# Optimization experiments

Hardware: AMD Instinct MI355X
Metric: run time of the kernel (lower is better)

The kernel has to match this reference:

```python
import jax, jax.numpy as jnp
import numpy as np
from jax import lax

A = 20          # alphabet size (input_size)
L = 512         # max_seq_length
CH = 8          # conv channels
N_LAYERS = 9    # log2(512) conv+pool stages


def setup_inputs() -> dict:
    key = jax.random.key(0)
    ks = jax.random.split(key, 6)
    B = 1024
    idx = jax.random.randint(ks[0], (B, L), 0, A)
    lens = jax.random.randint(ks[1], (B,), L // 4, L + 1)
    masks = jnp.arange(L)[None, :] < lens[:, None]            # [B, L] bool
    # one-hot sequences, zeroed at padded positions (so nonzero() skips them)
    x = jax.nn.one_hot(idx, A, dtype=jnp.float32) * masks[..., None].astype(jnp.float32)
    blosum = jax.random.normal(ks[2], (A, A), jnp.float32)
    blosum = (blosum + blosum.T) * 0.5                        # symmetric like BLOSUM
    lpm = blosum                                              # trainable copy
    pm = jnp.clip(blosum, 0.0)                                # clamp(min=0) constant
    std = jnp.ones((1,), jnp.float32)                         # Gaussian std for row decay
    w0 = jax.random.normal(ks[3], (CH, 1, 3), jnp.float32) * 0.3
    ws = jax.random.normal(ks[4], (N_LAYERS - 1, CH, CH, 3), jnp.float32) * 0.2
    return {"x": x, "masks": masks, "lpm": lpm, "pm": pm, "std": std, "w0": w0, "ws": ws}


def _shift_pos(m, k):
    # target index clamp(s + k, max=L-1): shift right by k, boundary index L-1
    # collects any source in the last k+1 positions (set semantics -> OR).
    head = jnp.zeros(m.shape[:-1] + (k,), dtype=bool)
    body = m[..., : L - k - 1]                                # targets k .. L-2
    last = jnp.any(m[..., L - 1 - k:], axis=-1, keepdims=True)
    return jnp.concatenate([head, body, last], axis=-1)


def _shift_neg(m, k):
    # target index clamp(s - k, min=0)
    first = jnp.any(m[..., : k + 1], axis=-1, keepdims=True)
    body = m[..., k + 1:]                                     # targets 1 .. L-1-k
    tail = jnp.zeros(m.shape[:-1] + (k,), dtype=bool)
    return jnp.concatenate([first, body, tail], axis=-1)


def _column(nz, lpm, pm):
    # Banded substitution scatter: each one-hot row i writes V[i, r] into row r
    # at the same (batch, seq) position. Original nested index_put loops collapse
    # to a single 20x20 matrix V applied via einsum (one-hot => no collisions).
    ii = jnp.arange(A)[:, None]
    rr = jnp.arange(A)[None, :]
    M = jnp.clip(lpm, 0.001, 1.0) * pm
    # up-writes: j in 1..18-i => i < r <= 18 ; down-writes: j in 1..i => r < i
    V = jnp.where((rr > ii) & (rr <= A - 2), M, 0.0) + jnp.where(rr < ii, M.T, 0.0)
    return jnp.einsum('bis,ir->brs', nz, V)


def _row(m, std):
    # Gaussian positional decay: writes exp(-k^2/(2 std^2)) at seq offsets +-k,
    # k = 1,2,3 in order (later k overwrites earlier at clamp collisions).
    row = jnp.zeros(m.shape, jnp.float32)
    for k in (1, 2, 3):
        mk = _shift_pos(m, k) | _shift_neg(m, k)
        vk = jnp.exp(-(k * k) / (2.0 * std * std))[0]
        row = jnp.where(mk, vk, row)
    return row


def _conv1d(h, w):
    # Conv1d(kernel=3, stride=1, pad=1, no bias)
    return lax.conv_general_dilated(h, w, (1,), [(1, 1)],
                                    dimension_numbers=('NCH', 'OIH', 'NCH'))


def _avgpool2(h):
    N, C, Lh = h.shape
    return h.reshape(N, C, Lh // 2, 2).mean(-1)


def reference(x, masks, lpm, pm, std, w0, ws):
    B = x.shape[0]
    xp = jnp.transpose(x, (0, 2, 1))          # [B, 20, L]
    m = xp != 0
    nz = m.astype(xp.dtype)
    h = xp + _column(nz, lpm, pm) + _row(m, std)
    h = h.reshape(B * A, 1, L)
    h = _avgpool2(_conv1d(h, w0))
    for i in range(N_LAYERS - 1):
        h = _avgpool2(_conv1d(h, ws[i]))
    return h.squeeze(-1).reshape(B, A, -1)    # [B, 20, 8]
```

## Files before the change

kernel.cpp:

```cpp
#include <hip/hip_runtime.h>
#include <math.h>

#define LSEQ 512
#define NA 20
#define NCH 8
#define SV 33

__global__ __launch_bounds__(256) void wf_vt_kernel(
    const float* __restrict__ w0,
    const float* __restrict__ wsg,
    const float* __restrict__ lpm,
    const float* __restrict__ pm,
    float* __restrict__ wf,
    float* __restrict__ vtn)
{
    const int t = threadIdx.x;

    if (blockIdx.x == NCH) {
        for (int o = t; o < NA * NA; o += 256) {
            int j = o / NA, a = o % NA;
            float v = 0.f;
            if (a > j && a <= NA - 2)
                v += fminf(fmaxf(lpm[j * NA + a], 0.001f), 1.0f) * pm[j * NA + a];
            if (a < j)
                v += fminf(fmaxf(lpm[a * NA + j], 0.001f), 1.0f) * pm[a * NA + j];
            vtn[o] = v;
        }
        return;
    }

    const int r = blockIdx.x;

    __shared__ float gA[NCH * 256];
    __shared__ float gB[NCH * 256];
    __shared__ float4 s_e[NCH * NCH];

    if (t < NCH) gA[t * 256] = (t == r) ? 1.f : 0.f;
    __syncthreads();

    int P = 1;
    for (int step = 0; step < 8; ++step) {
        const int li = 7 - step;
        if (t < 64) {
            const int co = t >> 3, ci = t & 7;
            const float* wp = wsg + li * 192 + co * 24 + ci * 3;
            const float a0 = wp[0], a1 = wp[1], a2 = wp[2];
            s_e[co * 8 + ci] = make_float4(a0 + a1, a2, a1 + a2, a0);
        }
        __syncthreads();
        const float* gi = (step & 1) ? gB : gA;
        float* go = (step & 1) ? gA : gB;
        for (int it = t; it < NCH * P; it += 256) {
            const int ci = it >> step;
            const int p = it & (P - 1);
            float accE = 0.f, accO = 0.f;
#pragma unroll
            for (int co = 0; co < NCH; ++co) {
                const float g0 = gi[co * 256 + p];
                const float gm = (p > 0) ? gi[co * 256 + p - 1] : 0.f;
                const float gp = (p + 1 < P) ? gi[co * 256 + p + 1] : 0.f;
                const float4 e = s_e[co * 8 + ci];
                accE += e.x * g0 + e.y * gm;
                accO += e.z * g0 + e.w * gp;
            }
            *(float2*)(go + ci * 256 + 2 * p) = make_float2(0.5f * accE, 0.5f * accO);
        }
        __syncthreads();
        P <<= 1;
    }

    {
        const int p = t;
        float accE = 0.f, accO = 0.f;
#pragma unroll
        for (int co = 0; co < NCH; ++co) {
            const float g0 = gA[co * 256 + p];
            const float gm = (p > 0) ? gA[co * 256 + p - 1] : 0.f;
            const float gp = (p < 255) ? gA[co * 256 + p + 1] : 0.f;
            const float q0 = w0[co * 3 + 0], q1 = w0[co * 3 + 1], q2 = w0[co * 3 + 2];
            accE += (q0 + q1) * g0 + q2 * gm;
            accO += (q1 + q2) * g0 + q0 * gp;
        }
        *(float2*)(wf + r * 512 + 2 * p) = make_float2(0.5f * accE, 0.5f * accO);
    }
}

#define BUILD_H(S_)                                                                     \
    do {                                                                                \
        const int s = (S_);                                                             \
        const int ai = s_idx[s];                                                        \
        const bool valid = ai < NA;                                                     \
        _Pragma("unroll")                                                               \
        for (int a = 0; a < NA; ++a) {                                                  \
            float v = valid ? (s_vtn[ai * SV + a] + (a == ai ? 1.f : 0.f)) : 0.f;       \
            s_h[a * 256 + t] = v;                                                       \
        }                                                                               \
        _Pragma("unroll")                                                               \
        for (int k = 1; k <= 3; ++k) {                                                  \
            const float add = (k == 1) ? vk1 : (k == 2) ? vk2 : vk3;                    \
            if (s == LSEQ - 1) {                                                        \
                for (int u = LSEQ - 1 - k; u <= LSEQ - 1; ++u) {                        \
                    int tg = s_idx[u];                                                  \
                    if (tg < NA)                                                        \
                        s_h[tg * 256 + t] =                                             \
                            (valid ? s_vtn[ai * SV + tg] + (tg == ai ? 1.f : 0.f) : 0.f) + add; \
                }                                                                       \
            } else if (s >= k) {                                                        \
                int tg = s_idx[s - k];                                                  \
                if (tg < NA)                                                            \
                    s_h[tg * 256 + t] =                                                 \
                        (valid ? s_vtn[ai * SV + tg] + (tg == ai ? 1.f : 0.f) : 0.f) + add; \
            }                                                                           \
            if (s == 0) {                                                               \
                for (int u = 0; u <= k; ++u) {                                          \
                    int tg = s_idx[u];                                                  \
                    if (tg < NA)                                                        \
                        s_h[tg * 256 + t] =                                             \
                            (valid ? s_vtn[ai * SV + tg] + (tg == ai ? 1.f : 0.f) : 0.f) + add; \
                }                                                                       \
            } else if (s + k < LSEQ) {                                                  \
                int tg = s_idx[s + k];                                                  \
                if (tg < NA)                                                            \
                    s_h[tg * 256 + t] =                                                 \
                        (valid ? s_vtn[ai * SV + tg] + (tg == ai ? 1.f : 0.f) : 0.f) + add; \
            }                                                                           \
        }                                                                               \
    } while (0)

#define PHASE2(WA_, WB_)                                                                \
    do {                                                                                \
        _Pragma("unroll 1")                                                             \
        for (int a = 0; a < NA; ++a) {                                                  \
            const float* hb = s_h + a * 256 + seg * 4;                                  \
            float4 h0 = *(const float4*)(hb);                                           \
            float4 h1 = *(const float4*)(hb + 128);                                     \
            float acc = h0.x * (WA_).x + h0.y * (WA_).y + h0.z * (WA_).z + h0.w * (WA_).w \
                      + h1.x * (WB_).x + h1.y * (WB_).y + h1.z * (WB_).z + h1.w * (WB_).w; \
            acc += __shfl_xor(acc, 8);                                                  \
            acc += __shfl_xor(acc, 16);                                                 \
            if ((lane & 24) == 0)                                                       \
                s_part[(w * 2 + (lane >> 5)) * (NA * NCH) + a * NCH + c] += acc;        \
        }                                                                               \
    } while (0)

__global__ __launch_bounds__(256, 4) void main_kernel(
    const float* __restrict__ x,
    const float* __restrict__ vtn,
    const float* __restrict__ g_std,
    const float* __restrict__ wf,
    float* __restrict__ out)
{
    const int b = blockIdx.x;
    const int t = threadIdx.x;
    const int c = t & 7;
    const int seg = t >> 3;
    const int w = t >> 6;
    const int lane = t & 63;

    __shared__ __align__(16) float s_h[NA * 256];
    __shared__ float s_vtn[NA * SV];
    __shared__ __align__(16) float s_part[8 * NA * NCH];
    __shared__ unsigned char s_idx[LSEQ];

    const float* wbase = wf + c * 512 + seg * 4;
    const float4 wr0 = *(const float4*)(wbase + 0);
    const float4 wr1 = *(const float4*)(wbase + 128);
    const float4 wr2 = *(const float4*)(wbase + 256);
    const float4 wr3 = *(const float4*)(wbase + 384);

    for (int i = t; i < NA * NA; i += 256) {
        int j = i / NA, a2 = i % NA;
        s_vtn[j * SV + a2] = vtn[i];
    }

    for (int i = t; i < 8 * NA * NCH / 4; i += 256) ((float4*)s_part)[i] = make_float4(0,0,0,0);

    const float4* xb = (const float4*)(x + (size_t)b * LSEQ * NA);
    {
        int id = 255;
#pragma unroll
        for (int q = 0; q < 5; ++q) {
            float4 v = xb[t * 5 + q];
            if (v.x > .5f) id = 4 * q + 0;
            if (v.y > .5f) id = 4 * q + 1;
            if (v.z > .5f) id = 4 * q + 2;
            if (v.w > .5f) id = 4 * q + 3;
        }
        s_idx[t] = (unsigned char)id;
    }
    if (t < 4) {
        int s = 256 + t;
        int id = 255;
#pragma unroll
        for (int q = 0; q < 5; ++q) {
            float4 v = xb[s * 5 + q];
            if (v.x > .5f) id = 4 * q + 0;
            if (v.y > .5f) id = 4 * q + 1;
            if (v.z > .5f) id = 4 * q + 2;
            if (v.w > .5f) id = 4 * q + 3;
        }
        s_idx[s] = (unsigned char)id;
    }
    __syncthreads();

    const float stdv = g_std[0];
    const float inv2s2 = 1.f / (2.f * stdv * stdv);
    const float vk1 = __expf(-1.f * inv2s2);
    const float vk2 = __expf(-4.f * inv2s2);
    const float vk3 = __expf(-9.f * inv2s2);

    BUILD_H(t);
    __syncthreads();

    const float4* xc = xb + (size_t)(t + 256) * 5;
    float4 xr0 = xc[0], xr1 = xc[1], xr2 = xc[2], xr3 = xc[3], xr4 = xc[4];

    PHASE2(wr0, wr1);

    {
        int id = 255;
        if (xr0.x > .5f) id = 0;
        if (xr0.y > .5f) id = 1;
        if (xr0.z > .5f) id = 2;
        if (xr0.w > .5f) id = 3;
        if (xr1.x > .5f) id = 4;
        if (xr1.y > .5f) id = 5;
        if (xr1.z > .5f) id = 6;
        if (xr1.w > .5f) id = 7;
        if (xr2.x > .5f) id = 8;
        if (xr2.y > .5f) id = 9;
        if (xr2.z > .5f) id = 10;
        if (xr2.w > .5f) id = 11;
        if (xr3.x > .5f) id = 12;
        if (xr3.y > .5f) id = 13;
        if (xr3.z > .5f) id = 14;
        if (xr3.w > .5f) id = 15;
        if (xr4.x > .5f) id = 16;
        if (xr4.y > .5f) id = 17;
        if (xr4.z > .5f) id = 18;
        if (xr4.w > .5f) id = 19;
        s_idx[256 + t] = (unsigned char)id;
    }
    __syncthreads();

    BUILD_H(256 + t);
    __syncthreads();

    PHASE2(wr2, wr3);
    __syncthreads();

    if (t < NA * NCH)
        out[(size_t)b * (NA * NCH) + t] =
            s_part[t]       + s_part[160 + t] + s_part[320 + t] + s_part[480 + t]
          + s_part[640 + t] + s_part[800 + t] + s_part[960 + t] + s_part[1120 + t];
}

extern "C" void kernel_launch(void* const* d_in, const int* in_sizes, int n_in,
                              void* d_out, int out_size, void* d_ws, size_t ws_size,
                              hipStream_t stream) {
    const float* x    = (const float*)d_in[0];
    const float* lpm  = (const float*)d_in[2];
    const float* pm   = (const float*)d_in[3];
    const float* stdp = (const float*)d_in[4];
    const float* w0   = (const float*)d_in[5];
    const float* wsg  = (const float*)d_in[6];
    float* out = (float*)d_out;

    const int B = in_sizes[0] / (LSEQ * NA);

    float* vtn = (float*)d_ws;
    float* wfb = (float*)d_ws + 1024;

    wf_vt_kernel<<<dim3(NCH + 1), dim3(256), 0, stream>>>(w0, wsg, lpm, pm, wfb, vtn);
    main_kernel<<<dim3(B), dim3(256), 0, stream>>>(x, vtn, stdp, wfb, out);
}
```

Before: 110.0 us.

## Restructure phase-2 contraction so each warp owns rows and reduces via shuffle transpose

```diff
diff --git a/kernel.cpp b/kernel.cpp
--- a/kernel.cpp
+++ b/kernel.cpp
@@ -5,6 +5,7 @@
 #define NA 20
 #define NCH 8
 #define SV 33
+#define PSTRIDE 168
 
 __global__ __launch_bounds__(256) void wf_vt_kernel(
     const float* __restrict__ w0,
@@ -127,20 +128,49 @@
         }                                                                               \
     } while (0)
 
-#define PHASE2(WA_, WB_)                                                                \
+#define DOT_ROW(J_, ACC_)                                                               \
     do {                                                                                \
-        _Pragma("unroll 1")                                                             \
-        for (int a = 0; a < NA; ++a) {                                                  \
-            const float* hb = s_h + a * 256 + seg * 4;                                  \
-            float4 h0 = *(const float4*)(hb);                                           \
-            float4 h1 = *(const float4*)(hb + 128);                                     \
-            float acc = h0.x * (WA_).x + h0.y * (WA_).y + h0.z * (WA_).z + h0.w * (WA_).w \
-                      + h1.x * (WB_).x + h1.y * (WB_).y + h1.z * (WB_).z + h1.w * (WB_).w; \
-            acc += __shfl_xor(acc, 8);                                                  \
-            acc += __shfl_xor(acc, 16);                                                 \
-            if ((lane & 24) == 0)                                                       \
-                s_part[(w * 2 + (lane >> 5)) * (NA * NCH) + a * NCH + c] += acc;        \
-        }                                                                               \
+        const float4 h = *(const float4*)(s_h + (w5 + (J_)) * 256 + 4 * lane);          \
+        float p0 = h.x * wc0.x + h.y * wc0.y + h.z * wc0.z + h.w * wc0.w;               \
+        float p1 = h.x * wc1.x + h.y * wc1.y + h.z * wc1.z + h.w * wc1.w;               \
+        float p2 = h.x * wc2.x + h.y * wc2.y + h.z * wc2.z + h.w * wc2.w;               \
+        float p3 = h.x * wc3.x + h.y * wc3.y + h.z * wc3.z + h.w * wc3.w;               \
+        float p4 = h.x * wc4.x + h.y * wc4.y + h.z * wc4.z + h.w * wc4.w;               \
+        float p5 = h.x * wc5.x + h.y * wc5.y + h.z * wc5.z + h.w * wc5.w;               \
+        float p6 = h.x * wc6.x + h.y * wc6.y + h.z * wc6.z + h.w * wc6.w;               \
+        float p7 = h.x * wc7.x + h.y * wc7.y + h.z * wc7.z + h.w * wc7.w;               \
+        float r0 = __shfl_xor(b1 ? p0 : p1, 1);                                         \
+        float r1 = __shfl_xor(b1 ? p2 : p3, 1);                                         \
+        float r2 = __shfl_xor(b1 ? p4 : p5, 1);                                         \
+        float r3 = __shfl_xor(b1 ? p6 : p7, 1);                                         \
+        float s0 = (b1 ? p1 : p0) + r0;                                                 \
+        float s1 = (b1 ? p3 : p2) + r1;                                                 \
+        float s2 = (b1 ? p5 : p4) + r2;                                                 \
+        float s3 = (b1 ? p7 : p6) + r3;                                                 \
+        float v0 = __shfl_xor(b2 ? s0 : s1, 2);                                         \
+        float v1 = __shfl_xor(b2 ? s2 : s3, 2);                                         \
+        float t0 = (b2 ? s1 : s0) + v0;                                                 \
+        float t1 = (b2 ? s3 : s2) + v1;                                                 \
+        float rz = __shfl_xor(b4 ? t0 : t1, 4);                                         \
+        (ACC_) += (b4 ? t1 : t0) + rz;                                                  \
+    } while (0)
+
+#define PHASE2H(HOFF_)                                                                  \
+    do {                                                                                \
+        const float* wfh = wf + (HOFF_) + 4 * lane;                                     \
+        const float4 wc0 = *(const float4*)(wfh + 0 * 512);                             \
+        const float4 wc1 = *(const float4*)(wfh + 1 * 512);                             \
+        const float4 wc2 = *(const float4*)(wfh + 2 * 512);                             \
+        const float4 wc3 = *(const float4*)(wfh + 3 * 512);                             \
+        const float4 wc4 = *(const float4*)(wfh + 4 * 512);                             \
+        const float4 wc5 = *(const float4*)(wfh + 5 * 512);                             \
+        const float4 wc6 = *(const float4*)(wfh + 6 * 512);                             \
+        const float4 wc7 = *(const float4*)(wfh + 7 * 512);                             \
+        DOT_ROW(0, acc0);                                                               \
+        DOT_ROW(1, acc1);                                                               \
+        DOT_ROW(2, acc2);                                                               \
+        DOT_ROW(3, acc3);                                                               \
+        DOT_ROW(4, acc4);                                                               \
     } while (0)
 
 __global__ __launch_bounds__(256, 4) void main_kernel(
@@ -152,44 +182,24 @@
 {
     const int b = blockIdx.x;
     const int t = threadIdx.x;
-    const int c = t & 7;
-    const int seg = t >> 3;
     const int w = t >> 6;
     const int lane = t & 63;
+    const int w5 = w * 5;
 
     __shared__ __align__(16) float s_h[NA * 256];
     __shared__ float s_vtn[NA * SV];
-    __shared__ __align__(16) float s_part[8 * NA * NCH];
+    __shared__ float s_part[8 * PSTRIDE];
     __shared__ unsigned char s_idx[LSEQ];
-
-    const float* wbase = wf + c * 512 + seg * 4;
-    const float4 wr0 = *(const float4*)(wbase + 0);
-    const float4 wr1 = *(const float4*)(wbase + 128);
-    const float4 wr2 = *(const float4*)(wbase + 256);
-    const float4 wr3 = *(const float4*)(wbase + 384);
 
     for (int i = t; i < NA * NA; i += 256) {
         int j = i / NA, a2 = i % NA;
         s_vtn[j * SV + a2] = vtn[i];
     }
 
-    for (int i = t; i < 8 * NA * NCH / 4; i += 256) ((float4*)s_part)[i] = make_float4(0,0,0,0);
-
     const float4* xb = (const float4*)(x + (size_t)b * LSEQ * NA);
-    {
-        int id = 255;
-#pragma unroll
-        for (int q = 0; q < 5; ++q) {
-            float4 v = xb[t * 5 + q];
-            if (v.x > .5f) id = 4 * q + 0;
-            if (v.y > .5f) id = 4 * q + 1;
-            if (v.z > .5f) id = 4 * q + 2;
-            if (v.w > .5f) id = 4 * q + 3;
-        }
-        s_idx[t] = (unsigned char)id;
-    }
-    if (t < 4) {
-        int s = 256 + t;
+#pragma unroll
+    for (int rep = 0; rep < 2; ++rep) {
+        int s = t + rep * 256;
         int id = 255;
 #pragma unroll
         for (int q = 0; q < 5; ++q) {
@@ -209,50 +219,36 @@
     const float vk2 = __expf(-4.f * inv2s2);
     const float vk3 = __expf(-9.f * inv2s2);
 
+    float acc0 = 0.f, acc1 = 0.f, acc2 = 0.f, acc3 = 0.f, acc4 = 0.f;
+    const bool b1 = lane & 1;
+    const bool b2 = lane & 2;
+    const bool b4 = lane & 4;
+
     BUILD_H(t);
     __syncthreads();
-
-    const float4* xc = xb + (size_t)(t + 256) * 5;
-    float4 xr0 = xc[0], xr1 = xc[1], xr2 = xc[2], xr3 = xc[3], xr4 = xc[4];
-
-    PHASE2(wr0, wr1);
+    PHASE2H(0);
+    __syncthreads();
+
+    BUILD_H(256 + t);
+    __syncthreads();
+    PHASE2H(256);
 
     {
-        int id = 255;
-        if (xr0.x > .5f) id = 0;
-        if (xr0.y > .5f) id = 1;
-        if (xr0.z > .5f) id = 2;
-        if (xr0.w > .5f) id = 3;
-        if (xr1.x > .5f) id = 4;
-        if (xr1.y > .5f) id = 5;
-        if (xr1.z > .5f) id = 6;
-        if (xr1.w > .5f) id = 7;
-        if (xr2.x > .5f) id = 8;
-        if (xr2.y > .5f) id = 9;
-        if (xr2.z > .5f) id = 10;
-        if (xr2.w > .5f) id = 11;
-        if (xr3.x > .5f) id = 12;
-        if (xr3.y > .5f) id = 13;
-        if (xr3.z > .5f) id = 14;
-        if (xr3.w > .5f) id = 15;
-        if (xr4.x > .5f) id = 16;
-        if (xr4.y > .5f) id = 17;
-        if (xr4.z > .5f) id = 18;
-        if (xr4.w > .5f) id = 19;
-        s_idx[256 + t] = (unsigned char)id;
-    }
-    __syncthreads();
-
-    BUILD_H(256 + t);
-    __syncthreads();
-
-    PHASE2(wr2, wr3);
+        const int base = (lane >> 3) * PSTRIDE + (lane & 7);
+        s_part[base + (w5 + 0) * 8] = acc0;
+        s_part[base + (w5 + 1) * 8] = acc1;
+        s_part[base + (w5 + 2) * 8] = acc2;
+        s_part[base + (w5 + 3) * 8] = acc3;
+        s_part[base + (w5 + 4) * 8] = acc4;
+    }
     __syncthreads();
 
     if (t < NA * NCH)
         out[(size_t)b * (NA * NCH) + t] =
-            s_part[t]       + s_part[160 + t] + s_part[320 + t] + s_part[480 + t]
-          + s_part[640 + t] + s_part[800 + t] + s_part[960 + t] + s_part[1120 + t];
+            s_part[0 * PSTRIDE + t] + s_part[1 * PSTRIDE + t]
+          + s_part[2 * PSTRIDE + t] + s_part[3 * PSTRIDE + t]
+          + s_part[4 * PSTRIDE + t] + s_part[5 * PSTRIDE + t]
+          + s_part[6 * PSTRIDE + t] + s_part[7 * PSTRIDE + t];
 }
 
 extern "C" void kernel_launch(void* const* d_in, const int* in_sizes, int n_in,
```

After: 107.4 us. 1.02x faster.
